# Kernel tuning notes

Hardware: AMD Instinct MI355X
Metric: run time of the kernel (lower is better)

The kernel has to match this reference:

```python
import jax, jax.numpy as jnp
import numpy as np

NUM_HEADS = 16

def _alibi(S, H, dtype):
    # fairseq-style ALiBi: slopes[h] * -(|i-j|), H assumed power of 2
    start = 2.0 ** (-8.0 / H)
    slopes = start ** jnp.arange(1, H + 1, dtype=jnp.float32)      # [H]
    pos = jnp.arange(S)
    rel = -jnp.abs(pos[None, :] - pos[:, None]).astype(jnp.float32)  # [S,S]
    return (slopes[:, None, None] * rel).astype(dtype)             # [H,S,S]

def setup_inputs() -> dict:
    key = jax.random.key(0)
    kx, km, kw1, kw2 = jax.random.split(key, 4)
    B, S, D = 2, 2048, 1024
    inputs = jax.random.normal(kx, (B, S, D), dtype=jnp.float32)
    mask = jax.random.bernoulli(km, 0.9, (B, S))
    mask = mask.at[:, 0].set(True)  # ensure each row has a valid key
    Wqkv = jax.random.normal(kw1, (3 * D, D), dtype=jnp.float32) * 0.02
    bqkv = jnp.zeros((3 * D,), dtype=jnp.float32)
    Wproj = jax.random.normal(kw2, (D, D), dtype=jnp.float32) * 0.02
    bproj = jnp.zeros((D,), dtype=jnp.float32)
    return {"inputs": inputs, "mask": mask, "Wqkv": Wqkv, "bqkv": bqkv,
            "Wproj": Wproj, "bproj": bproj}

def reference(inputs, mask, Wqkv, bqkv, Wproj, bproj):
    B, S, D = inputs.shape
    H = NUM_HEADS
    dh = D // H
    scale = D ** (-0.5)  # NOTE: original scales by full dim, not head dim
    qkv = inputs @ Wqkv.T + bqkv                       # [B,S,3D]
    qkv = qkv.reshape(B, S, H, 3 * dh).transpose(0, 2, 1, 3)  # [B,H,S,3dh]
    q, k, v = qkv[..., :dh], qkv[..., dh:2 * dh], qkv[..., 2 * dh:]
    attn = jnp.einsum('bhqd,bhkd->bhqk', q, k) * scale  # [B,H,S,S]
    attn = attn + _alibi(S, H, attn.dtype)[None]
    attn = jnp.where(mask[:, None, None, :], attn, jnp.finfo(attn.dtype).min)
    attn = jax.nn.softmax(attn, axis=-1)
    x = jnp.einsum('bhqk,bhkd->bhqd', attn, v)          # [B,H,S,dh]
    x = x.transpose(0, 2, 1, 3).reshape(B, S, D)
    return x @ Wproj.T + bproj
```

## Files before the change

### kernel.cpp

```cpp
#include <hip/hip_runtime.h>
#include <cstdint>
#include <cstddef>

#define B_  2
#define S_  2048
#define D_  1024
#define H_  16
#define DH_ 64
#define M_  (B_*S_)
#define N3_ (3*D_)
#define NT_ (S_/64)

typedef float f32x4 __attribute__((ext_vector_type(4)));
typedef short short8 __attribute__((ext_vector_type(8)));
typedef unsigned short u16x8 __attribute__((ext_vector_type(8)));
typedef unsigned short u16x4 __attribute__((ext_vector_type(4)));
typedef unsigned short u16x2 __attribute__((ext_vector_type(2)));

__device__ __forceinline__ unsigned short f2bf(float x) {
    unsigned int u = __float_as_uint(x);
    unsigned int r = (u + 0x7FFFu + ((u >> 16) & 1u)) >> 16;
    return (unsigned short)r;
}

__device__ __forceinline__ float exp2_(float x) { return __builtin_amdgcn_exp2f(x); }

__device__ __forceinline__ unsigned int cvt_pk_bf16(float a, float b) {
    unsigned int r;
    asm volatile("v_cvt_pk_bf16_f32 %0, %1, %2" : "=v"(r) : "v"(a), "v"(b));
    return r;
}

__device__ __forceinline__ int xcd_swizzle(int lin, int nwg) {
    const int cpx = nwg >> 3;
    return (lin & 7) * cpx + (lin >> 3);
}

__device__ __forceinline__ void gload16(const void* g, void* l) {
    __builtin_amdgcn_global_load_lds(
        (const __attribute__((address_space(1))) unsigned int*)g,
        (__attribute__((address_space(3))) unsigned int*)l,
        16, 0, 0);
}

__global__ void k_detect_mask(const unsigned char* __restrict__ mb, int* __restrict__ flag) {
    __shared__ int sBig, sM4, sM8;
    if (threadIdx.x == 0) { sBig = 0; sM4 = 0; sM8 = 0; }
    __syncthreads();
    int big = 0, m4 = 0, m8 = 0;
    for (int i = threadIdx.x; i < 4096; i += blockDim.x) {
        unsigned char v = mb[i];
        if (v > 1) big = 1;
        if (v && (i & 3)) m4 = 1;
        if (v && ((i & 7) == 4)) m8 = 1;
    }
    if (big) atomicOr(&sBig, 1);
    if (m4)  atomicOr(&sM4, 1);
    if (m8)  atomicOr(&sM8, 1);
    __syncthreads();
    if (threadIdx.x == 0) {
        int w;
        if (sBig)      w = 0;
        else if (sM4)  w = 1;
        else if (sM8)  w = 4;
        else           w = 8;
        *flag = w;
    }
}

__global__ void k_expand_mask(const void* __restrict__ mask, const int* __restrict__ flag,
                              float* __restrict__ maskbias, int n) {
    int i = blockIdx.x * blockDim.x + threadIdx.x;
    if (i >= n) return;
    int w = *flag;
    bool on;
    if (w == 0)      on = ((const float*)mask)[i] != 0.0f;
    else if (w == 1) on = ((const unsigned char*)mask)[i] != 0;
    else if (w == 4) on = ((const int*)mask)[i] != 0;
    else             on = ((const long long*)mask)[i] != 0;
    maskbias[i] = on ? 0.0f : -1e30f;
}

__global__ void k_f2bf3(const float* __restrict__ A, const float* __restrict__ B2,
                        const float* __restrict__ C, unsigned short* __restrict__ oA,
                        unsigned short* __restrict__ oB, unsigned short* __restrict__ oC) {
    const int nA = M_ * D_, nB = N3_ * D_, nC = D_ * D_;
    int i = (blockIdx.x * 256 + threadIdx.x) * 4;
    const float* src; unsigned short* dst; int off;
    if (i < nA)           { src = A;  dst = oA; off = i; }
    else if (i < nA + nB) { src = B2; dst = oB; off = i - nA; }
    else if (i < nA + nB + nC) { src = C; dst = oC; off = i - nA - nB; }
    else return;
    float4 v = *reinterpret_cast<const float4*>(&src[off]);
    u16x4 o = { f2bf(v.x), f2bf(v.y), f2bf(v.z), f2bf(v.w) };
    *reinterpret_cast<u16x4*>(&dst[off]) = o;
}

template <bool OUT_BF16>
__global__ __launch_bounds__(256) void k_gemm_bf16_nt(
    const unsigned short* __restrict__ A, const unsigned short* __restrict__ W,
    const float* __restrict__ bias, void* __restrict__ Cout,
    int M, int N, int K) {
    __shared__ __align__(16) unsigned short Al[128 * 64];
    __shared__ __align__(16) unsigned short Wl[128 * 64];

    const int tid  = threadIdx.x;
    const int lane = tid & 63;
    const int w    = tid >> 6;
    const int wr   = w >> 1, wc = w & 1;
    const int l16  = lane & 15, g = lane >> 4;
    const int m0 = blockIdx.y * 128, n0 = blockIdx.x * 128;

    f32x4 acc[4][4];
#pragma unroll
    for (int m = 0; m < 4; ++m)
#pragma unroll
        for (int n = 0; n < 4; ++n) acc[m][n] = (f32x4){0.f, 0.f, 0.f, 0.f};

    const int srow = tid >> 3, scol = (tid & 7) * 8;

    for (int k0 = 0; k0 < K; k0 += 64) {
        __syncthreads();
#pragma unroll
        for (int i = 0; i < 4; ++i) {
            const int c = i * 256 + tid;
            const int row = srow + i * 32;
            gload16(A + (size_t)(m0 + row) * K + k0 + scol, Al + c * 8);
            gload16(W + (size_t)(n0 + row) * K + k0 + scol, Wl + c * 8);
        }
        __syncthreads();

#pragma unroll
        for (int kk = 0; kk < 2; ++kk) {
            short8 a[4], b[4];
#pragma unroll
            for (int m = 0; m < 4; ++m)
                a[m] = *reinterpret_cast<const short8*>(
                    &Al[(size_t)(wr * 64 + m * 16 + l16) * 64 + kk * 32 + g * 8]);
#pragma unroll
            for (int n = 0; n < 4; ++n)
                b[n] = *reinterpret_cast<const short8*>(
                    &Wl[(size_t)(wc * 64 + n * 16 + l16) * 64 + kk * 32 + g * 8]);
#pragma unroll
            for (int m = 0; m < 4; ++m)
#pragma unroll
                for (int n = 0; n < 4; ++n)
                    acc[m][n] = __builtin_amdgcn_mfma_f32_16x16x32_bf16(a[m], b[n], acc[m][n], 0, 0, 0);
        }
    }

    float bv[4];
#pragma unroll
    for (int n = 0; n < 4; ++n) bv[n] = bias[n0 + wc * 64 + n * 16 + l16];
#pragma unroll
    for (int m = 0; m < 4; ++m) {
#pragma unroll
        for (int r = 0; r < 4; ++r) {
            const size_t row = m0 + wr * 64 + m * 16 + g * 4 + r;
#pragma unroll
            for (int n = 0; n < 4; ++n) {
                const int col = n0 + wc * 64 + n * 16 + l16;
                float v = acc[m][n][r] + bv[n];
                if (OUT_BF16)
                    ((unsigned short*)Cout)[row * N + col] = f2bf(v);
                else
                    ((float*)Cout)[row * N + col] = v;
            }
        }
    }
}

__global__ __launch_bounds__(512, 4) void k_attn_mfma(
    const unsigned short* __restrict__ qkv,
    const float* __restrict__ maskbias,
    unsigned short* __restrict__ x) {
    __shared__ __align__(16) unsigned short Kt[2][64][72];
    __shared__ __align__(16) unsigned short Vt[3][64][72];
    __shared__ __align__(16) unsigned short QP[128][72];

    const int tid  = threadIdx.x;
    const int lane = tid & 63;
    const int wq   = tid >> 6;
    const int g    = lane >> 4;
    const int g4   = g * 4;
    const int l16  = lane & 15;

    const int nqt = S_ / 128;
    const int nwg = B_ * H_ * nqt;
    const int bid = xcd_swizzle(blockIdx.x, nwg);
    const int qt = bid % nqt;
    const int h  = (bid / nqt) % H_;
    const int b  = bid / (nqt * H_);
    const int q0 = qt * 128;
    const size_t rowbase = (size_t)b * S_ * N3_;
    const int hq = h * 192, hk = hq + 64, hv = hq + 128;
    const unsigned short* kvb = qkv + rowbase;
    const float* mbp = maskbias + b * S_;

    {
        const int row = tid >> 2, cb = (tid & 3) * 16;
        const unsigned short* src = kvb + (size_t)(q0 + row) * N3_ + hq + cb;
        *reinterpret_cast<u16x8*>(&QP[row][cb])     = *reinterpret_cast<const u16x8*>(src);
        *reinterpret_cast<u16x8*>(&QP[row][cb + 8]) = *reinterpret_cast<const u16x8*>(src + 8);
    }

    const int krow = tid >> 3, kcb = (tid & 7) * 8;
    const int vkb = (tid & 31) * 2, vdb = (tid >> 5) * 4;
    u16x8 kr;
    u16x4 vr0, vr1;

    {
        kr  = *reinterpret_cast<const u16x8*>(kvb + (size_t)krow * N3_ + hk + kcb);
        const unsigned short* vs = kvb + (size_t)vkb * N3_ + hv + vdb;
        vr0 = *reinterpret_cast<const u16x4*>(vs);
        vr1 = *reinterpret_cast<const u16x4*>(vs + N3_);
        *reinterpret_cast<u16x8*>(&Kt[0][krow][kcb]) = kr;
#pragma unroll
        for (int j = 0; j < 4; ++j)
            *reinterpret_cast<u16x2*>(&Vt[0][vdb + j][vkb]) = (u16x2){vr0[j], vr1[j]};
    }
    __syncthreads();

    const short8 qa0 = *reinterpret_cast<const short8*>(&QP[wq*16 + l16][g*8]);
    const short8 qa1 = *reinterpret_cast<const short8*>(&QP[wq*16 + l16][32 + g*8]);

    f32x4 Oacc[4];
#pragma unroll
    for (int df = 0; df < 4; ++df) Oacc[df] = (f32x4){0.f, 0.f, 0.f, 0.f};
    float m = -1e30f, l = 0.0f;

    const float LOG2E = 1.4426950408889634f;
    const float c1 = 0.03125f * LOG2E;
    const float c2 = exp2f(-0.5f * (float)(h + 1)) * LOG2E;
    const int   qw0 = q0 + wq * 16;
    const int   qg  = qw0 + l16;
    float albr[4];
#pragma unroll
    for (int r = 0; r < 4; ++r) albr[r] = c2 * (float)(g4 + r);
    const float c2_16 = c2 * 16.0f;

    float p_[4][4];

    {
        kr  = *reinterpret_cast<const u16x8*>(kvb + (size_t)(64 + krow) * N3_ + hk + kcb);
        const unsigned short* vs = kvb + (size_t)(64 + vkb) * N3_ + hv + vdb;
        vr0 = *reinterpret_cast<const u16x4*>(vs);
        vr1 = *reinterpret_cast<const u16x4*>(vs + N3_);

        __builtin_amdgcn_s_setprio(1);
#pragma unroll
        for (int jb = 0; jb < 4; ++jb) {
            short8 kb0 = *reinterpret_cast<const short8*>(&Kt[0][jb*16 + l16][g*8]);
            short8 kb1 = *reinterpret_cast<const short8*>(&Kt[0][jb*16 + l16][32 + g*8]);
            f32x4 c = (f32x4){0.f, 0.f, 0.f, 0.f};
            c = __builtin_amdgcn_mfma_f32_16x16x32_bf16(kb0, qa0, c, 0, 0, 0);
            c = __builtin_amdgcn_mfma_f32_16x16x32_bf16(kb1, qa1, c, 0, 0, 0);
#pragma unroll
            for (int r = 0; r < 4; ++r) p_[jb][r] = c[r];
        }
        __builtin_amdgcn_s_setprio(0);

        *reinterpret_cast<u16x8*>(&Kt[1][krow][kcb]) = kr;
#pragma unroll
        for (int j = 0; j < 4; ++j)
            *reinterpret_cast<u16x2*>(&Vt[1][vdb + j][vkb]) = (u16x2){vr0[j], vr1[j]};
    }
    __syncthreads();
    {
        kr  = *reinterpret_cast<const u16x8*>(kvb + (size_t)(128 + krow) * N3_ + hk + kcb);
        const unsigned short* vs = kvb + (size_t)(128 + vkb) * N3_ + hv + vdb;
        vr0 = *reinterpret_cast<const u16x4*>(vs);
        vr1 = *reinterpret_cast<const u16x4*>(vs + N3_);
    }

    int vb_r = 0;
    int vb_w = 2;

    for (int t = 1; t < NT_ + 1; ++t) {
        const int k0m = (t - 1) * 64;

        f32x4 amv[4];
#pragma unroll
        for (int jb = 0; jb < 4; ++jb)
            amv[jb] = *reinterpret_cast<const f32x4*>(&mbp[k0m + jb * 16 + g4]);

        f32x4 cnx[4];
        if (t < NT_) {
            const unsigned short (*Kc)[72] = Kt[t & 1];
            __builtin_amdgcn_s_setprio(1);
#pragma unroll
            for (int jb = 0; jb < 4; ++jb) {
                short8 kb0 = *reinterpret_cast<const short8*>(&Kc[jb*16 + l16][g*8]);
                short8 kb1 = *reinterpret_cast<const short8*>(&Kc[jb*16 + l16][32 + g*8]);
                f32x4 c = (f32x4){0.f, 0.f, 0.f, 0.f};
                c = __builtin_amdgcn_mfma_f32_16x16x32_bf16(kb0, qa0, c, 0, 0, 0);
                c = __builtin_amdgcn_mfma_f32_16x16x32_bf16(kb1, qa1, c, 0, 0, 0);
                cnx[jb] = c;
            }
            __builtin_amdgcn_s_setprio(0);
        }

        if (k0m + 64 <= qw0) {
            const float tb = c2 * (float)(k0m - qg);
#pragma unroll
            for (int jb = 0; jb < 4; ++jb) {
                const float tbj = tb + c2_16 * (float)jb;
#pragma unroll
                for (int r = 0; r < 4; ++r)
                    p_[jb][r] = fmaf(p_[jb][r], c1, tbj + albr[r] + amv[jb][r]);
            }
        } else if (k0m >= qw0 + 16) {
            const float tb = c2 * (float)(k0m - qg);
#pragma unroll
            for (int jb = 0; jb < 4; ++jb) {
                const float tbj = -tb - c2_16 * (float)jb;
#pragma unroll
                for (int r = 0; r < 4; ++r)
                    p_[jb][r] = fmaf(p_[jb][r], c1, tbj - albr[r] + amv[jb][r]);
            }
        } else {
            const int dbase = k0m - qg;
#pragma unroll
            for (int jb = 0; jb < 4; ++jb)
#pragma unroll
                for (int r = 0; r < 4; ++r) {
                    int d = dbase + jb * 16 + g4 + r;
                    d = d < 0 ? -d : d;
                    p_[jb][r] = fmaf(p_[jb][r], c1, amv[jb][r] - c2 * (float)d);
                }
        }

        float mx;
        {
            float m0_ = fmaxf(fmaxf(p_[0][0], p_[0][1]), fmaxf(p_[0][2], p_[0][3]));
            float m1_ = fmaxf(fmaxf(p_[1][0], p_[1][1]), fmaxf(p_[1][2], p_[1][3]));
            float m2_ = fmaxf(fmaxf(p_[2][0], p_[2][1]), fmaxf(p_[2][2], p_[2][3]));
            float m3_ = fmaxf(fmaxf(p_[3][0], p_[3][1]), fmaxf(p_[3][2], p_[3][3]));
            mx = fmaxf(fmaxf(m0_, m1_), fmaxf(m2_, m3_));
        }
        mx = fmaxf(mx, __shfl_xor(mx, 16));
        mx = fmaxf(mx, __shfl_xor(mx, 32));

        if (__any(mx > m + 8.0f)) {
            const float mn = fmaxf(m, mx);
            const float cr = exp2_(m - mn);
            m = mn;
            l *= cr;
            const int srcb = (lane & 48) + ((lane & 48) >> 2);
#pragma unroll
            for (int r = 0; r < 4; ++r) {
                const float crq = __shfl(cr, srcb + r);
#pragma unroll
                for (int df = 0; df < 4; ++df) Oacc[df][r] *= crq;
            }
        }

        float ps = 0.0f;
#pragma unroll
        for (int jb = 0; jb < 4; ++jb)
#pragma unroll
            for (int r = 0; r < 4; ++r) {
                float p = exp2_(p_[jb][r] - m);
                p_[jb][r] = p;
                ps += p;
            }

#pragma unroll
        for (int jb = 0; jb < 4; ++jb) {
            uint2 st;
            st.x = cvt_pk_bf16(p_[jb][0], p_[jb][1]);
            st.y = cvt_pk_bf16(p_[jb][2], p_[jb][3]);
            *reinterpret_cast<uint2*>(&QP[wq*16 + l16][jb*16 + g4]) = st;
        }

        {
            const short8 pa0 = *reinterpret_cast<const short8*>(&QP[wq*16 + l16][g*8]);
            const short8 pa1 = *reinterpret_cast<const short8*>(&QP[wq*16 + l16][32 + g*8]);
            const unsigned short (*Vc)[72] = Vt[vb_r];
            __builtin_amdgcn_s_setprio(1);
#pragma unroll
            for (int df = 0; df < 4; ++df) {
                short8 vb0 = *reinterpret_cast<const short8*>(&Vc[df*16 + l16][g*8]);
                short8 vb1 = *reinterpret_cast<const short8*>(&Vc[df*16 + l16][32 + g*8]);
                Oacc[df] = __builtin_amdgcn_mfma_f32_16x16x32_bf16(pa0, vb0, Oacc[df], 0, 0, 0);
                Oacc[df] = __builtin_amdgcn_mfma_f32_16x16x32_bf16(pa1, vb1, Oacc[df], 0, 0, 0);
            }
            __builtin_amdgcn_s_setprio(0);
        }

        ps += __shfl_xor(ps, 16);
        ps += __shfl_xor(ps, 32);
        l += ps;

        if (t + 1 < NT_) {
            *reinterpret_cast<u16x8*>(&Kt[(t + 1) & 1][krow][kcb]) = kr;
#pragma unroll
            for (int j = 0; j < 4; ++j)
                *reinterpret_cast<u16x2*>(&Vt[vb_w][vdb + j][vkb]) = (u16x2){vr0[j], vr1[j]};
            __syncthreads();
            if (t + 2 < NT_) {
                const int kn = (t + 2) * 64;
                kr  = *reinterpret_cast<const u16x8*>(kvb + (size_t)(kn + krow) * N3_ + hk + kcb);
                const unsigned short* vs = kvb + (size_t)(kn + vkb) * N3_ + hv + vdb;
                vr0 = *reinterpret_cast<const u16x4*>(vs);
                vr1 = *reinterpret_cast<const u16x4*>(vs + N3_);
            }
        }
        vb_r = (vb_r == 2) ? 0 : vb_r + 1;
        vb_w = (vb_w == 2) ? 0 : vb_w + 1;

        if (t < NT_) {
#pragma unroll
            for (int jb = 0; jb < 4; ++jb)
#pragma unroll
                for (int r = 0; r < 4; ++r) p_[jb][r] = cnx[jb][r];
        }
    }

    const int srcb = (lane & 48) + ((lane & 48) >> 2);
    float invq[4];
#pragma unroll
    for (int r = 0; r < 4; ++r) invq[r] = 1.0f / __shfl(l, srcb + r);
#pragma unroll
    for (int df = 0; df < 4; ++df) {
#pragma unroll
        for (int r = 0; r < 4; ++r) {
            const int qrow = q0 + wq * 16 + g4 + r;
            x[(size_t)(b * S_ + qrow) * D_ + h * 64 + df * 16 + l16] = f2bf(Oacc[df][r] * invq[r]);
        }
    }
}

extern "C" void kernel_launch(void* const* d_in, const int* in_sizes, int n_in,
                              void* d_out, int out_size, void* d_ws, size_t ws_size,
                              hipStream_t stream) {
    const float* inputs = (const float*)d_in[0];
    const void*  mask   = d_in[1];
    const float* Wqkv   = (const float*)d_in[2];
    const float* bqkv   = (const float*)d_in[3];
    const float* Wproj  = (const float*)d_in[4];
    const float* bproj  = (const float*)d_in[5];
    float* out = (float*)d_out;

    unsigned short* qkvb = (unsigned short*)d_ws;
    unsigned short* xb   = qkvb + (size_t)M_ * N3_;
    unsigned short* Ab   = xb + (size_t)M_ * D_;
    unsigned short* Wqb  = Ab + (size_t)M_ * D_;
    unsigned short* Wpb  = Wqb + (size_t)N3_ * D_;
    float* maskbias = (float*)(Wpb + (size_t)D_ * D_);
    int*   flag     = (int*)(maskbias + M_);

    k_detect_mask<<<1, 256, 0, stream>>>((const unsigned char*)mask, flag);
    k_expand_mask<<<(M_ + 255) / 256, 256, 0, stream>>>(mask, flag, maskbias, M_);

    const int ntot = M_ * D_ + N3_ * D_ + D_ * D_;
    k_f2bf3<<<(ntot / 4 + 255) / 256, 256, 0, stream>>>(inputs, Wqkv, Wproj, Ab, Wqb, Wpb);

    dim3 g1(N3_ / 128, M_ / 128);
    k_gemm_bf16_nt<true><<<g1, 256, 0, stream>>>(Ab, Wqb, bqkv, qkvb, M_, N3_, D_);

    k_attn_mfma<<<B_ * H_ * (S_ / 128), 512, 0, stream>>>(qkvb, maskbias, xb);

    dim3 g2(D_ / 128, M_ / 128);
    k_gemm_bf16_nt<false><<<g2, 256, 0, stream>>>(xb, Wpb, bproj, out, M_, D_, D_);
}
```

Measured before the change: 173.2 us.

## Triple-buffer GEMM tiles with async loads, XOR swizzle, and 8 waves per block

Rewrites both bf16 GEMMs to use a three-stage LDS ring. Tiles are prefetched two k-steps ahead, and explicit vmcnt waits let global loads overlap MFMA work instead of using a full sync-load-sync per step. LDS columns get an XOR swizzle to cut bank conflicts, and the block grows to 512 threads (8 waves, each holding a 64x32 accumulator tile), with setprio raised around the MFMA section. The cost is triple the LDS (96KB), which may limit occupancy, and the correctness now depends on hand-written waitcnt counts matching the number of loads issued.

```diff
diff --git a/kernel.cpp b/kernel.cpp
--- a/kernel.cpp
+++ b/kernel.cpp
@@ -97,69 +97,101 @@
 }
 
 template <bool OUT_BF16>
-__global__ __launch_bounds__(256) void k_gemm_bf16_nt(
+__global__ __launch_bounds__(512) void k_gemm_bf16_cv(
     const unsigned short* __restrict__ A, const unsigned short* __restrict__ W,
     const float* __restrict__ bias, void* __restrict__ Cout,
     int M, int N, int K) {
-    __shared__ __align__(16) unsigned short Al[128 * 64];
-    __shared__ __align__(16) unsigned short Wl[128 * 64];
+    __shared__ __align__(16) unsigned short Al[3][128 * 64];
+    __shared__ __align__(16) unsigned short Wl[3][128 * 64];
 
     const int tid  = threadIdx.x;
     const int lane = tid & 63;
     const int w    = tid >> 6;
-    const int wr   = w >> 1, wc = w & 1;
+    const int wr   = w >> 2, wc = w & 3;
     const int l16  = lane & 15, g = lane >> 4;
     const int m0 = blockIdx.y * 128, n0 = blockIdx.x * 128;
-
-    f32x4 acc[4][4];
+    const int NTk = K >> 6;
+
+    f32x4 acc[4][2];
 #pragma unroll
     for (int m = 0; m < 4; ++m)
 #pragma unroll
-        for (int n = 0; n < 4; ++n) acc[m][n] = (f32x4){0.f, 0.f, 0.f, 0.f};
-
-    const int srow = tid >> 3, scol = (tid & 7) * 8;
-
-    for (int k0 = 0; k0 < K; k0 += 64) {
-        __syncthreads();
-#pragma unroll
-        for (int i = 0; i < 4; ++i) {
-            const int c = i * 256 + tid;
-            const int row = srow + i * 32;
-            gload16(A + (size_t)(m0 + row) * K + k0 + scol, Al + c * 8);
-            gload16(W + (size_t)(n0 + row) * K + k0 + scol, Wl + c * 8);
-        }
-        __syncthreads();
-
-#pragma unroll
-        for (int kk = 0; kk < 2; ++kk) {
-            short8 a[4], b[4];
+        for (int n = 0; n < 2; ++n) acc[m][n] = (f32x4){0.f, 0.f, 0.f, 0.f};
+
+    auto issueTile = [&](int kt) {
+        const int k0 = kt << 6;
+        unsigned short* Ad = Al[kt % 3];
+        unsigned short* Wd = Wl[kt % 3];
+#pragma unroll
+        for (int i = 0; i < 2; ++i) {
+            const int c = i * 512 + tid;
+            const int row = c >> 3;
+            const int colel = (((c & 7) ^ (row & 7)) << 3);
+            gload16(A + (size_t)(m0 + row) * K + k0 + colel, Ad + c * 8);
+            gload16(W + (size_t)(n0 + row) * K + k0 + colel, Wd + c * 8);
+        }
+    };
+
+    issueTile(0);
+    issueTile(1);
+
+    for (int t = 0; t < NTk; ++t) {
+        if (t + 2 < NTk) issueTile(t + 2);
+
+        if (t < NTk - 2)       asm volatile("s_waitcnt vmcnt(8)" ::: "memory");
+        else if (t == NTk - 2) asm volatile("s_waitcnt vmcnt(4)" ::: "memory");
+        else                   asm volatile("s_waitcnt vmcnt(0)" ::: "memory");
+        __builtin_amdgcn_s_barrier();
+        __builtin_amdgcn_sched_barrier(0);
+
+        const unsigned short* Ab = Al[t % 3];
+        const unsigned short* Wb = Wl[t % 3];
+        short8 a[4][2], b[2][2];
+#pragma unroll
+        for (int m = 0; m < 4; ++m)
+#pragma unroll
+            for (int kk = 0; kk < 2; ++kk) {
+                const int row = wr * 64 + m * 16 + l16;
+                const int kb = (kk * 64 + g * 16) ^ ((row & 7) << 4);
+                a[m][kk] = *reinterpret_cast<const short8*>(
+                    (const char*)Ab + row * 128 + kb);
+            }
+#pragma unroll
+        for (int n = 0; n < 2; ++n)
+#pragma unroll
+            for (int kk = 0; kk < 2; ++kk) {
+                const int row = wc * 32 + n * 16 + l16;
+                const int kb = (kk * 64 + g * 16) ^ ((row & 7) << 4);
+                b[n][kk] = *reinterpret_cast<const short8*>(
+                    (const char*)Wb + row * 128 + kb);
+            }
+
+        __builtin_amdgcn_s_setprio(1);
+#pragma unroll
+        for (int kk = 0; kk < 2; ++kk)
 #pragma unroll
             for (int m = 0; m < 4; ++m)
-                a[m] = *reinterpret_cast<const short8*>(
-                    &Al[(size_t)(wr * 64 + m * 16 + l16) * 64 + kk * 32 + g * 8]);
-#pragma unroll
-            for (int n = 0; n < 4; ++n)
-                b[n] = *reinterpret_cast<const short8*>(
-                    &Wl[(size_t)(wc * 64 + n * 16 + l16) * 64 + kk * 32 + g * 8]);
-#pragma unroll
-            for (int m = 0; m < 4; ++m)
-#pragma unroll
-                for (int n = 0; n < 4; ++n)
-                    acc[m][n] = __builtin_amdgcn_mfma_f32_16x16x32_bf16(a[m], b[n], acc[m][n], 0, 0, 0);
-        }
-    }
-
-    float bv[4];
-#pragma unroll
-    for (int n = 0; n < 4; ++n) bv[n] = bias[n0 + wc * 64 + n * 16 + l16];
+#pragma unroll
+                for (int n = 0; n < 2; ++n)
+                    acc[m][n] = __builtin_amdgcn_mfma_f32_16x16x32_bf16(
+                        a[m][kk], b[n][kk], acc[m][n], 0, 0, 0);
+        __builtin_amdgcn_s_setprio(0);
+
+        __builtin_amdgcn_sched_barrier(0);
+        __builtin_amdgcn_s_barrier();
+    }
+
+    float bv[2];
+#pragma unroll
+    for (int n = 0; n < 2; ++n) bv[n] = bias[n0 + wc * 32 + n * 16 + l16];
 #pragma unroll
     for (int m = 0; m < 4; ++m) {
 #pragma unroll
         for (int r = 0; r < 4; ++r) {
             const size_t row = m0 + wr * 64 + m * 16 + g * 4 + r;
 #pragma unroll
-            for (int n = 0; n < 4; ++n) {
-                const int col = n0 + wc * 64 + n * 16 + l16;
+            for (int n = 0; n < 2; ++n) {
+                const int col = n0 + wc * 32 + n * 16 + l16;
                 float v = acc[m][n][r] + bv[n];
                 if (OUT_BF16)
                     ((unsigned short*)Cout)[row * N + col] = f2bf(v);
@@ -457,10 +489,10 @@
     k_f2bf3<<<(ntot / 4 + 255) / 256, 256, 0, stream>>>(inputs, Wqkv, Wproj, Ab, Wqb, Wpb);
 
     dim3 g1(N3_ / 128, M_ / 128);
-    k_gemm_bf16_nt<true><<<g1, 256, 0, stream>>>(Ab, Wqb, bqkv, qkvb, M_, N3_, D_);
+    k_gemm_bf16_cv<true><<<g1, 512, 0, stream>>>(Ab, Wqb, bqkv, qkvb, M_, N3_, D_);
 
     k_attn_mfma<<<B_ * H_ * (S_ / 128), 512, 0, stream>>>(qkvb, maskbias, xb);
 
     dim3 g2(D_ / 128, M_ / 128);
-    k_gemm_bf16_nt<false><<<g2, 256, 0, stream>>>(xb, Wpb, bproj, out, M_, D_, D_);
-}
+    k_gemm_bf16_cv<false><<<g2, 512, 0, stream>>>(xb, Wpb, bproj, out, M_, D_, D_);
+}
```

After: 166.0 us. 4.1% less time.
